# Kernel tuning notes

Measured on AMD Instinct MI355X. Metric: run time of the kernel, lower is better.

Reference implementation:

```python
import jax, jax.numpy as jnp
import numpy as np

HEADS = 16


def setup_inputs() -> dict:
    key = jax.random.key(0)
    ks = jax.random.split(key, 5)
    n, s, d = 2, 2048, 1024
    return {
        "x": jax.random.normal(ks[0], (n, s, d), dtype=jnp.float32),
        "Wqkv": jax.random.normal(ks[1], (3 * d, d), dtype=jnp.float32) * (d ** -0.5),
        "bqkv": jax.random.normal(ks[2], (3 * d,), dtype=jnp.float32) * 0.02,
        "Wd": jax.random.normal(ks[3], (d, d), dtype=jnp.float32) * (d ** -0.5),
        "bd": jax.random.normal(ks[4], (d,), dtype=jnp.float32) * 0.02,
        "mask": 1,
    }


def reference(x, Wqkv, bqkv, Wd, bd, mask):
    n, s, d = x.shape
    h = HEADS
    hd = d // h
    qkv = x @ Wqkv.T + bqkv  # [n, s, 3d]
    q, k, v = jnp.split(qkv, 3, axis=-1)
    # [n, h, s, hd]
    q = q.reshape(n, s, h, hd).transpose(0, 2, 1, 3)
    k = k.reshape(n, s, h, hd).transpose(0, 2, 1, 3)
    v = v.reshape(n, s, h, hd).transpose(0, 2, 1, 3)
    scores = jnp.einsum("bhqd,bhkd->bhqk", q, k)
    if mask:
        causal = jnp.triu(jnp.ones((s, s), dtype=bool), k=1)
        scores = jnp.where(causal, -jnp.inf, scores)
    attn = jax.nn.softmax(scores / jnp.sqrt(jnp.float32(hd)), axis=-1)
    out = jnp.einsum("bhqk,bhkd->bhqd", attn, v)
    out = out.transpose(0, 2, 1, 3).reshape(n, s, d)
    return out @ Wd.T + bd
```

## Files before the change

### kernel.cpp

```cpp
#include <hip/hip_runtime.h>
#include <hip/hip_bf16.h>
#include <cstdint>
#include <cstddef>

typedef __attribute__((ext_vector_type(8))) short bf8_t;
typedef __attribute__((ext_vector_type(4))) float f4_t;

__device__ __forceinline__ unsigned short f2bf(float f) {
    union { float f; unsigned int u; } v; v.f = f;
    unsigned int u = v.u + 0x7FFFu + ((v.u >> 16) & 1u);
    return (unsigned short)(u >> 16);
}

__device__ __forceinline__ void gl_lds16(const void* g, void* l) {
    __builtin_amdgcn_global_load_lds(
        (const __attribute__((address_space(1))) unsigned int*)g,
        (__attribute__((address_space(3))) unsigned int*)l,
        16, 0, 0);
}

__global__ void cvt_kernel(const float* __restrict__ src, unsigned short* __restrict__ dst, int n4) {
    int i = blockIdx.x * blockDim.x + threadIdx.x;
    if (i >= n4) return;
    float4 f = ((const float4*)src)[i];
    ushort4 o;
    o.x = f2bf(f.x); o.y = f2bf(f.y); o.z = f2bf(f.z); o.w = f2bf(f.w);
    ((ushort4*)dst)[i] = o;
}

template<int MODE>
__global__ __launch_bounds__(256, 2) void gemm_bt_kernel(
    const unsigned short* __restrict__ A,
    const unsigned short* __restrict__ W,
    const float* __restrict__ bias,
    float* __restrict__ outf,
    unsigned short* __restrict__ qb,
    unsigned short* __restrict__ kb,
    unsigned short* __restrict__ vtb,
    int K, int Nn)
{
    __shared__ unsigned short As[128][32];
    __shared__ unsigned short Bs[128][32];

    const int tid  = threadIdx.x;
    const int lane = tid & 63;
    const int w    = tid >> 6;
    const int wm   = w & 1;
    const int wn   = w >> 1;
    const int quad = lane >> 4;
    const int l16  = lane & 15;
    const int m0   = blockIdx.y * 128;
    const int n0   = blockIdx.x * 128;

    const int lrow = lane >> 2;
    const int lcol = (lane & 3) << 3;

    f4_t acc[4][4];
    {
        f4_t z = {0.f, 0.f, 0.f, 0.f};
        #pragma unroll
        for (int i = 0; i < 4; ++i)
            #pragma unroll
            for (int j = 0; j < 4; ++j) acc[i][j] = z;
    }

    const unsigned short* Ag0 = A + (size_t)(m0 + w * 16 + lrow) * K + lcol;
    const unsigned short* Ag1 = A + (size_t)(m0 + 64 + w * 16 + lrow) * K + lcol;
    const unsigned short* Bg0 = W + (size_t)(n0 + w * 16 + lrow) * K + lcol;
    const unsigned short* Bg1 = W + (size_t)(n0 + 64 + w * 16 + lrow) * K + lcol;
    unsigned short* lA0 = &As[w * 16][0];
    unsigned short* lA1 = &As[64 + w * 16][0];
    unsigned short* lB0 = &Bs[w * 16][0];
    unsigned short* lB1 = &Bs[64 + w * 16][0];

    for (int kk = 0; kk < K; kk += 32) {
        __syncthreads();
        gl_lds16(Ag0 + kk, lA0);
        gl_lds16(Ag1 + kk, lA1);
        gl_lds16(Bg0 + kk, lB0);
        gl_lds16(Bg1 + kk, lB1);
        __syncthreads();

        bf8_t af[4], bfr[4];
        #pragma unroll
        for (int mb = 0; mb < 4; ++mb)
            af[mb] = *(const bf8_t*)&As[wm * 64 + mb * 16 + l16][quad * 8];
        #pragma unroll
        for (int nb = 0; nb < 4; ++nb)
            bfr[nb] = *(const bf8_t*)&Bs[wn * 64 + nb * 16 + l16][quad * 8];
        #pragma unroll
        for (int mb = 0; mb < 4; ++mb)
            #pragma unroll
            for (int nb = 0; nb < 4; ++nb)
                acc[mb][nb] = __builtin_amdgcn_mfma_f32_16x16x32_bf16(af[mb], bfr[nb], acc[mb][nb], 0, 0, 0);
    }

    #pragma unroll
    for (int nb = 0; nb < 4; ++nb) {
        const int col = n0 + wn * 64 + nb * 16 + l16;
        const float bc = bias[col];
        const int which  = col >> 10;
        const int within = col & 1023;
        const int head   = within >> 6;
        const int hdi    = within & 63;
        #pragma unroll
        for (int mb = 0; mb < 4; ++mb) {
            #pragma unroll
            for (int r = 0; r < 4; ++r) {
                const int row = m0 + wm * 64 + mb * 16 + quad * 4 + r;
                const float v = acc[mb][nb][r] + bc;
                if (MODE == 0) {
                    const int b  = row >> 11;
                    const int sq = row & 2047;
                    const int bh = b * 16 + head;
                    const unsigned short bv = f2bf(v);
                    if (which == 0)      qb [((size_t)bh * 2048 + sq) * 64 + hdi] = bv;
                    else if (which == 1) kb [((size_t)bh * 2048 + sq) * 64 + hdi] = bv;
                    else                 vtb[((size_t)bh * 64 + hdi) * 2048 + sq] = bv;
                } else {
                    outf[(size_t)row * Nn + col] = v;
                }
            }
        }
    }
}

__global__ __launch_bounds__(256, 4) void attn_kernel(
    const unsigned short* __restrict__ qg,
    const unsigned short* __restrict__ kg,
    const unsigned short* __restrict__ vg,
    unsigned short* __restrict__ ao)
{
    __shared__ unsigned short QP[64][72];
    __shared__ unsigned short Ks[64][72];
    __shared__ unsigned short Vs[64][72];

    const int tid  = threadIdx.x;
    const int lane = tid & 63;
    const int w    = tid >> 6;
    const int quad = lane >> 4;
    const int l16  = lane & 15;
    const int bh   = blockIdx.y;
    const int qt   = (blockIdx.x + blockIdx.y) & 31;
    const int q0   = qt * 64;
    const int b    = bh >> 4;
    const int head = bh & 15;

    const unsigned short* Qp = qg + (size_t)bh * 2048 * 64;
    const unsigned short* Kp = kg + (size_t)bh * 2048 * 64;
    const unsigned short* Vp = vg + (size_t)bh * 64 * 2048;

    const int sr = tid >> 2;
    const int sc = (tid & 3) << 4;

    {
        float4 a = *(const float4*)(Qp + (size_t)(q0 + sr) * 64 + sc);
        float4 c = *(const float4*)(Qp + (size_t)(q0 + sr) * 64 + sc + 8);
        *(float4*)&QP[sr][sc]     = a;
        *(float4*)&QP[sr][sc + 8] = c;
    }
    bf8_t aq[2];
    aq[0] = *(const bf8_t*)&QP[w * 16 + l16][quad * 8];
    aq[1] = *(const bf8_t*)&QP[w * 16 + l16][32 + quad * 8];

    bf8_t bones;
    {
        const short one = (l16 == 0) ? (short)0x3F80 : (short)0;
        #pragma unroll
        for (int j = 0; j < 8; ++j) bones[j] = one;
    }

    f4_t oacc[4];
    f4_t lacc;
    {
        f4_t z = {0.f, 0.f, 0.f, 0.f};
        #pragma unroll
        for (int j = 0; j < 4; ++j) oacc[j] = z;
        lacc = z;
    }

    const int nkt = qt + 1;

    float4 k0 = *(const float4*)(Kp + (size_t)sr * 64 + sc);
    float4 k1 = *(const float4*)(Kp + (size_t)sr * 64 + sc + 8);
    float4 v0 = *(const float4*)(Vp + (size_t)sr * 2048 + sc);
    float4 v1 = *(const float4*)(Vp + (size_t)sr * 2048 + sc + 8);

    for (int kt = 0; kt < nkt; ++kt) {
        __syncthreads();
        *(float4*)&Ks[sr][sc]     = k0;
        *(float4*)&Ks[sr][sc + 8] = k1;
        *(float4*)&Vs[sr][sc]     = v0;
        *(float4*)&Vs[sr][sc + 8] = v1;
        __syncthreads();

        if (kt + 1 < nkt) {
            const int sk = (kt + 1) << 6;
            k0 = *(const float4*)(Kp + (size_t)(sk + sr) * 64 + sc);
            k1 = *(const float4*)(Kp + (size_t)(sk + sr) * 64 + sc + 8);
            v0 = *(const float4*)(Vp + (size_t)sr * 2048 + sk + sc);
            v1 = *(const float4*)(Vp + (size_t)sr * 2048 + sk + sc + 8);
        }

        f4_t sacc[4];
        {
            f4_t z = {0.f, 0.f, 0.f, 0.f};
            #pragma unroll
            for (int j = 0; j < 4; ++j) sacc[j] = z;
        }
        #pragma unroll
        for (int ks = 0; ks < 2; ++ks) {
            #pragma unroll
            for (int nb = 0; nb < 4; ++nb) {
                bf8_t bk = *(const bf8_t*)&Ks[nb * 16 + l16][ks * 32 + quad * 8];
                sacc[nb] = __builtin_amdgcn_mfma_f32_16x16x32_bf16(aq[ks], bk, sacc[nb], 0, 0, 0);
            }
        }

        const bool diag = (kt == nkt - 1);
        #pragma unroll
        for (int r = 0; r < 4; ++r) {
            const int rloc = (w << 4) + (quad << 2) + r;
            #pragma unroll
            for (int nb = 0; nb < 4; ++nb) {
                float s = fmaf(sacc[nb][r], 0.125f, -14.0f);
                if (diag && (nb * 16 + l16 > rloc)) s = -1e30f;
                union { float f; unsigned int u; } pv;
                pv.f = __expf(s);
                QP[rloc][nb * 16 + l16] = (unsigned short)(pv.u >> 16);
            }
        }

        #pragma unroll
        for (int ks = 0; ks < 2; ++ks) {
            bf8_t ap = *(const bf8_t*)&QP[(w << 4) + l16][ks * 32 + quad * 8];
            #pragma unroll
            for (int nb = 0; nb < 4; ++nb) {
                bf8_t bv = *(const bf8_t*)&Vs[nb * 16 + l16][ks * 32 + quad * 8];
                oacc[nb] = __builtin_amdgcn_mfma_f32_16x16x32_bf16(ap, bv, oacc[nb], 0, 0, 0);
            }
            lacc = __builtin_amdgcn_mfma_f32_16x16x32_bf16(ap, bones, lacc, 0, 0, 0);
        }
    }

    #pragma unroll
    for (int r = 0; r < 4; ++r) {
        const float lsum = __shfl(lacc[r], lane & 48);
        const float rl = 1.f / lsum;
        const int sq = q0 + (w << 4) + (quad << 2) + r;
        #pragma unroll
        for (int nb = 0; nb < 4; ++nb) {
            const int dcol = head * 64 + nb * 16 + l16;
            ao[((size_t)(b * 2048 + sq)) * 1024 + dcol] = f2bf(oacc[nb][r] * rl);
        }
    }
}

extern "C" void kernel_launch(void* const* d_in, const int* in_sizes, int n_in,
                              void* d_out, int out_size, void* d_ws, size_t ws_size,
                              hipStream_t stream) {
    const float* x    = (const float*)d_in[0];
    const float* Wqkv = (const float*)d_in[1];
    const float* bqkv = (const float*)d_in[2];
    const float* Wd   = (const float*)d_in[3];
    const float* bd   = (const float*)d_in[4];
    float* out = (float*)d_out;

    char* ws = (char*)d_ws;
    unsigned short* xb    = (unsigned short*)(ws);
    unsigned short* wqkvb = (unsigned short*)(ws + 8388608);
    unsigned short* wdb   = (unsigned short*)(ws + 14680064);
    unsigned short* qb2   = (unsigned short*)(ws + 16777216);
    unsigned short* kb2   = (unsigned short*)(ws + 25165824);
    unsigned short* vtb   = (unsigned short*)(ws + 33554432);
    unsigned short* ao    = xb;

    cvt_kernel<<<4096, 256, 0, stream>>>(x,    xb,    1048576);
    cvt_kernel<<<3072, 256, 0, stream>>>(Wqkv, wqkvb, 786432);
    cvt_kernel<<<1024, 256, 0, stream>>>(Wd,   wdb,   262144);

    gemm_bt_kernel<0><<<dim3(24, 32), 256, 0, stream>>>(
        xb, wqkvb, bqkv, nullptr, qb2, kb2, vtb, 1024, 3072);

    attn_kernel<<<dim3(32, 32), 256, 0, stream>>>(qb2, kb2, vtb, ao);

    gemm_bt_kernel<1><<<dim3(8, 32), 256, 0, stream>>>(
        ao, wdb, bd, out, nullptr, nullptr, nullptr, 1024, 1024);
}
```

Before: 205.2 us.

## Pair causal query tiles per block and double-buffer K/V in shared memory

Each attention block now handles two query tiles (tiles 31-j and j), so every block processes 33 key tiles and the causal work is balanced, while the grid is halved. K/V shared tiles are double-buffered, which removes one barrier per iteration. The exponent is folded into exp2f with prescaled constants. Occupancy bounds drop from 4 to 2 blocks per CU and LDS use grows, and with only 512 blocks the achievable latency hiding may be lower.

```diff
diff --git a/kernel.cpp b/kernel.cpp
--- a/kernel.cpp
+++ b/kernel.cpp
@@ -125,15 +125,15 @@
     }
 }
 
-__global__ __launch_bounds__(256, 4) void attn_kernel(
+__global__ __launch_bounds__(256, 2) void attn_kernel(
     const unsigned short* __restrict__ qg,
     const unsigned short* __restrict__ kg,
     const unsigned short* __restrict__ vg,
     unsigned short* __restrict__ ao)
 {
     __shared__ unsigned short QP[64][72];
-    __shared__ unsigned short Ks[64][72];
-    __shared__ unsigned short Vs[64][72];
+    __shared__ unsigned short Ks[2][64][72];
+    __shared__ unsigned short Vs[2][64][72];
 
     const int tid  = threadIdx.x;
     const int lane = tid & 63;
@@ -141,8 +141,9 @@
     const int quad = lane >> 4;
     const int l16  = lane & 15;
     const int bh   = blockIdx.y;
-    const int qt   = (blockIdx.x + blockIdx.y) & 31;
-    const int q0   = qt * 64;
+    const int jj   = blockIdx.x;
+    const int qtBig   = 31 - jj;
+    const int qtSmall = jj;
     const int b    = bh >> 4;
     const int head = bh & 15;
 
@@ -153,12 +154,18 @@
     const int sr = tid >> 2;
     const int sc = (tid & 3) << 4;
 
-    {
-        float4 a = *(const float4*)(Qp + (size_t)(q0 + sr) * 64 + sc);
-        float4 c = *(const float4*)(Qp + (size_t)(q0 + sr) * 64 + sc + 8);
-        *(float4*)&QP[sr][sc]     = a;
-        *(float4*)&QP[sr][sc + 8] = c;
-    }
+    float4 q0a = *(const float4*)(Qp + (size_t)(qtBig * 64 + sr) * 64 + sc);
+    float4 q0b = *(const float4*)(Qp + (size_t)(qtBig * 64 + sr) * 64 + sc + 8);
+    float4 q1a = *(const float4*)(Qp + (size_t)(qtSmall * 64 + sr) * 64 + sc);
+    float4 q1b = *(const float4*)(Qp + (size_t)(qtSmall * 64 + sr) * 64 + sc + 8);
+
+    float4 k0 = *(const float4*)(Kp + (size_t)sr * 64 + sc);
+    float4 k1 = *(const float4*)(Kp + (size_t)sr * 64 + sc + 8);
+    float4 v0 = *(const float4*)(Vp + (size_t)sr * 2048 + sc);
+    float4 v1 = *(const float4*)(Vp + (size_t)sr * 2048 + sc + 8);
+
+    *(float4*)&QP[sr][sc]     = q0a;
+    *(float4*)&QP[sr][sc + 8] = q0b;
     bf8_t aq[2];
     aq[0] = *(const bf8_t*)&QP[w * 16 + l16][quad * 8];
     aq[1] = *(const bf8_t*)&QP[w * 16 + l16][32 + quad * 8];
@@ -179,28 +186,55 @@
         lacc = z;
     }
 
-    const int nkt = qt + 1;
-
-    float4 k0 = *(const float4*)(Kp + (size_t)sr * 64 + sc);
-    float4 k1 = *(const float4*)(Kp + (size_t)sr * 64 + sc + 8);
-    float4 v0 = *(const float4*)(Vp + (size_t)sr * 2048 + sc);
-    float4 v1 = *(const float4*)(Vp + (size_t)sr * 2048 + sc + 8);
-
-    for (int kt = 0; kt < nkt; ++kt) {
+    auto epilogue = [&](int qt) {
+        #pragma unroll
+        for (int r = 0; r < 4; ++r) {
+            const float lsum = __shfl(lacc[r], lane & 48);
+            const float rl = 1.f / lsum;
+            const int sq = qt * 64 + (w << 4) + (quad << 2) + r;
+            #pragma unroll
+            for (int nb = 0; nb < 4; ++nb) {
+                const int dcol = head * 64 + nb * 16 + l16;
+                ao[((size_t)(b * 2048 + sq)) * 1024 + dcol] = f2bf(oacc[nb][r] * rl);
+            }
+        }
+    };
+
+    const int p0len = 32 - jj;
+
+    for (int t = 0; t < 33; ++t) {
+        const int buf = t & 1;
+        *(float4*)&Ks[buf][sr][sc]     = k0;
+        *(float4*)&Ks[buf][sr][sc + 8] = k1;
+        *(float4*)&Vs[buf][sr][sc]     = v0;
+        *(float4*)&Vs[buf][sr][sc + 8] = v1;
         __syncthreads();
-        *(float4*)&Ks[sr][sc]     = k0;
-        *(float4*)&Ks[sr][sc + 8] = k1;
-        *(float4*)&Vs[sr][sc]     = v0;
-        *(float4*)&Vs[sr][sc + 8] = v1;
-        __syncthreads();
-
-        if (kt + 1 < nkt) {
-            const int sk = (kt + 1) << 6;
-            k0 = *(const float4*)(Kp + (size_t)(sk + sr) * 64 + sc);
-            k1 = *(const float4*)(Kp + (size_t)(sk + sr) * 64 + sc + 8);
+
+        if (t + 1 < 33) {
+            const int t2 = t + 1;
+            const size_t sk = (size_t)((t2 >= p0len) ? (t2 - p0len) : t2) << 6;
+            k0 = *(const float4*)(Kp + (sk + sr) * 64 + sc);
+            k1 = *(const float4*)(Kp + (sk + sr) * 64 + sc + 8);
             v0 = *(const float4*)(Vp + (size_t)sr * 2048 + sk + sc);
             v1 = *(const float4*)(Vp + (size_t)sr * 2048 + sk + sc + 8);
         }
+
+        if (t == p0len) {
+            epilogue(qtBig);
+            f4_t z = {0.f, 0.f, 0.f, 0.f};
+            #pragma unroll
+            for (int j = 0; j < 4; ++j) oacc[j] = z;
+            lacc = z;
+            *(float4*)&QP[sr][sc]     = q1a;
+            *(float4*)&QP[sr][sc + 8] = q1b;
+            aq[0] = *(const bf8_t*)&QP[w * 16 + l16][quad * 8];
+            aq[1] = *(const bf8_t*)&QP[w * 16 + l16][32 + quad * 8];
+        }
+
+        const bool ph1 = (t >= p0len);
+        const int  kt  = ph1 ? (t - p0len) : t;
+        const int  qt  = ph1 ? qtSmall : qtBig;
+        const bool diag = (kt == qt);
 
         f4_t sacc[4];
         {
@@ -212,21 +246,20 @@
         for (int ks = 0; ks < 2; ++ks) {
             #pragma unroll
             for (int nb = 0; nb < 4; ++nb) {
-                bf8_t bk = *(const bf8_t*)&Ks[nb * 16 + l16][ks * 32 + quad * 8];
+                bf8_t bk = *(const bf8_t*)&Ks[buf][nb * 16 + l16][ks * 32 + quad * 8];
                 sacc[nb] = __builtin_amdgcn_mfma_f32_16x16x32_bf16(aq[ks], bk, sacc[nb], 0, 0, 0);
             }
         }
 
-        const bool diag = (kt == nkt - 1);
         #pragma unroll
         for (int r = 0; r < 4; ++r) {
             const int rloc = (w << 4) + (quad << 2) + r;
             #pragma unroll
             for (int nb = 0; nb < 4; ++nb) {
-                float s = fmaf(sacc[nb][r], 0.125f, -14.0f);
-                if (diag && (nb * 16 + l16 > rloc)) s = -1e30f;
+                float e = fmaf(sacc[nb][r], 0.18033688f, -20.197731f);
+                if (diag && (nb * 16 + l16 > rloc)) e = -1e30f;
                 union { float f; unsigned int u; } pv;
-                pv.f = __expf(s);
+                pv.f = exp2f(e);
                 QP[rloc][nb * 16 + l16] = (unsigned short)(pv.u >> 16);
             }
         }
@@ -236,24 +269,14 @@
             bf8_t ap = *(const bf8_t*)&QP[(w << 4) + l16][ks * 32 + quad * 8];
             #pragma unroll
             for (int nb = 0; nb < 4; ++nb) {
-                bf8_t bv = *(const bf8_t*)&Vs[nb * 16 + l16][ks * 32 + quad * 8];
+                bf8_t bv = *(const bf8_t*)&Vs[buf][nb * 16 + l16][ks * 32 + quad * 8];
                 oacc[nb] = __builtin_amdgcn_mfma_f32_16x16x32_bf16(ap, bv, oacc[nb], 0, 0, 0);
             }
             lacc = __builtin_amdgcn_mfma_f32_16x16x32_bf16(ap, bones, lacc, 0, 0, 0);
         }
     }
 
-    #pragma unroll
-    for (int r = 0; r < 4; ++r) {
-        const float lsum = __shfl(lacc[r], lane & 48);
-        const float rl = 1.f / lsum;
-        const int sq = q0 + (w << 4) + (quad << 2) + r;
-        #pragma unroll
-        for (int nb = 0; nb < 4; ++nb) {
-            const int dcol = head * 64 + nb * 16 + l16;
-            ao[((size_t)(b * 2048 + sq)) * 1024 + dcol] = f2bf(oacc[nb][r] * rl);
-        }
-    }
+    epilogue(qtSmall);
 }
 
 extern "C" void kernel_launch(void* const* d_in, const int* in_sizes, int n_in,
@@ -282,7 +305,7 @@
     gemm_bt_kernel<0><<<dim3(24, 32), 256, 0, stream>>>(
         xb, wqkvb, bqkv, nullptr, qb2, kb2, vtb, 1024, 3072);
 
-    attn_kernel<<<dim3(32, 32), 256, 0, stream>>>(qb2, kb2, vtb, ao);
+    attn_kernel<<<dim3(16, 32), 256, 0, stream>>>(qb2, kb2, vtb, ao);
 
     gemm_bt_kernel<1><<<dim3(8, 32), 256, 0, stream>>>(
         ao, wdb, bd, out, nullptr, nullptr, nullptr, 1024, 1024);
```

After: 202.5 us. Within noise of the previous version (-1.3%).
